# Kernel optimization log

Hardware: AMD Instinct MI355X
Metric: run time of the kernel (lower is better)

## Reference

```python
import jax, jax.numpy as jnp
import numpy as np
from jax import lax

# --- static config (matches init_kwargs) ---
K_NAT, P_NAT, NHEAD, DM, L = 5, 2, 8, 128, 3
PK, OV, STRIDE = 4, 2, 2          # patcher kernel / overlap / stride = PK-OV
PPAD = PK - OV                    # circular pad for patcher/depatcher crop
RK, RC = 5, 12                    # res layer kernel, hidden channels = 3*4
DN = ('NCHW', 'OIHW', 'NCHW')


def setup_inputs() -> dict:
    key = jax.random.key(0)
    ks = jax.random.split(key, 16)
    B, C, H, W = 2, 3, 256, 256
    rn = lambda k, shape, s=0.02: jax.random.normal(k, shape, jnp.float32) * s
    return {
        'x': jax.random.normal(ks[0], (B, C, H, W), jnp.float32),
        'pos_w': jax.random.uniform(ks[1], (C, H, W), jnp.float32) + 0.5,
        'pos_b': jax.random.uniform(ks[2], (C, H, W), jnp.float32) - 0.5,
        'patch_w': rn(ks[3], (DM, C, PK, PK), 0.05),
        'patch_b': jnp.zeros((DM,), jnp.float32),
        'ln1_g': jnp.ones((L, DM), jnp.float32),
        'ln1_b': jnp.zeros((L, DM), jnp.float32),
        'qkv_w': rn(ks[4], (L, 3 * DM, DM)),
        'qkv_b': jnp.zeros((L, 3 * DM), jnp.float32),
        'rpb': rn(ks[5], (L, NHEAD, 2 * K_NAT - 1, 2 * K_NAT - 1)),
        'proj_w': rn(ks[6], (L, DM, DM)),
        'proj_b': jnp.zeros((L, DM), jnp.float32),
        'ln2_g': jnp.ones((L, DM), jnp.float32),
        'ln2_b': jnp.zeros((L, DM), jnp.float32),
        'fc1_w': rn(ks[7], (L, 4 * DM, DM)),
        'fc1_b': jnp.zeros((L, 4 * DM), jnp.float32),
        'fc2_w': rn(ks[8], (L, DM, 4 * DM)),
        'fc2_b': jnp.zeros((L, DM), jnp.float32),
        'depatch_w': rn(ks[9], (DM, C, PK, PK), 0.05),   # ConvTranspose2d weight (Cin,Cout,kh,kw)
        'depatch_b': jnp.zeros((C,), jnp.float32),
        'res_cv1_w': rn(ks[10], (RC, C, RK, RK), 0.05),
        'res_cv1_b': jnp.zeros((RC,), jnp.float32),
        'res_cv2_w': rn(ks[11], (C, RC, 1, 1), 0.05),
        'res_cv2_b': jnp.zeros((C,), jnp.float32),
    }


def _layer_norm(x, g, b):
    m = x.mean(-1, keepdims=True)
    v = x.var(-1, keepdims=True)
    return (x - m) * lax.rsqrt(v + 1e-5) * g + b


def _nat_block(x, ln1_g, ln1_b, qkv_w, qkv_b, rpb, proj_w, proj_b,
               ln2_g, ln2_b, fc1_w, fc1_b, fc2_w, fc2_b):
    # x: (B,H,W,C). NATLayer: LN -> circular pad by k//2 -> NA -> crop -> residual -> LN -> MLP -> residual.
    # After padding, every kept (interior) pixel has a full centered kxk neighborhood,
    # so we compute q only at interior positions and gather kxk K/V windows from the padded map.
    B, H, W, C = x.shape
    k, p, h = K_NAT, P_NAT, NHEAD
    dh = C // h
    y = _layer_norm(x, ln1_g, ln1_b)
    y = jnp.pad(y, ((0, 0), (p, p), (p, p), (0, 0)), mode='wrap')  # circular
    qkv = y @ qkv_w.T + qkv_b                                      # (B,H+2p,W+2p,3C)
    q, kk, vv = jnp.split(qkv, 3, axis=-1)
    q = q[:, p:p + H, p:p + W].reshape(B, H, W, h, dh) * (dh ** -0.5)
    def win(t):
        t = t.reshape(B, H + 2 * p, W + 2 * p, h, dh)
        return jnp.stack([t[:, i:i + H, j:j + W]
                          for i in range(k) for j in range(k)], axis=3)  # (B,H,W,k*k,h,dh)
    kw, vw = win(kk), win(vv)
    bias = rpb[:, p:p + k, p:p + k].reshape(h, k * k)  # centered slice of (2k-1,2k-1) RPB
    logits = jnp.einsum('bxyhd,bxynhd->bxyhn', q, kw) + bias
    a = jax.nn.softmax(logits, axis=-1)
    o = jnp.einsum('bxyhn,bxynhd->bxyhd', a, vw).reshape(B, H, W, C)
    x = x + (o @ proj_w.T + proj_b)
    y = _layer_norm(x, ln2_g, ln2_b)
    y = jax.nn.leaky_relu(y @ fc1_w.T + fc1_b) @ fc2_w.T + fc2_b
    return x + y


def _forward(x, pos_w, pos_b, patch_w, patch_b, ln1_g, ln1_b, qkv_w, qkv_b,
             rpb, proj_w, proj_b, ln2_g, ln2_b, fc1_w, fc1_b, fc2_w, fc2_b,
             depatch_w, depatch_b, res_cv1_w, res_cv1_b, res_cv2_w, res_cv2_b):
    # positional embedding (dropout is identity, p=0)
    x = x * pos_w + pos_b
    # OverlapConvPatcher: circular pad by (PK-OV), conv kernel PK stride PK-OV -> (B,129,129,DM)
    xp = jnp.pad(x, ((0, 0), (0, 0), (PPAD, PPAD), (PPAD, PPAD)), mode='wrap')
    f = lax.conv_general_dilated(xp, patch_w, (STRIDE, STRIDE), 'VALID',
                                 dimension_numbers=DN) + patch_b[None, :, None, None]
    f = f.transpose(0, 2, 3, 1)
    for i in range(L):
        f = _nat_block(f, ln1_g[i], ln1_b[i], qkv_w[i], qkv_b[i], rpb[i],
                       proj_w[i], proj_b[i], ln2_g[i], ln2_b[i],
                       fc1_w[i], fc1_b[i], fc2_w[i], fc2_b[i])
    # OverlapDeconvDepatcher: ConvTranspose2d (kernel PK, stride PK-OV), crop PPAD border
    f = f.transpose(0, 3, 1, 2)
    wf = jnp.flip(depatch_w, (2, 3)).transpose(1, 0, 2, 3)  # (Cout,Cin,kh,kw)
    y = lax.conv_general_dilated(f, wf, (1, 1), [(PK - 1, PK - 1)] * 2,
                                 lhs_dilation=(STRIDE, STRIDE),
                                 dimension_numbers=DN) + depatch_b[None, :, None, None]
    y = y[:, :, PPAD:-PPAD, PPAD:-PPAD]  # (B,3,256,256)
    # ResLayer: circular-pad same conv 5x5 -> leaky_relu -> 1x1 conv -> residual
    yp = jnp.pad(y, ((0, 0), (0, 0), (RK // 2, RK // 2), (RK // 2, RK // 2)), mode='wrap')
    r = lax.conv_general_dilated(yp, res_cv1_w, (1, 1), 'VALID',
                                 dimension_numbers=DN) + res_cv1_b[None, :, None, None]
    r = jax.nn.leaky_relu(r)
    r = lax.conv_general_dilated(r, res_cv2_w, (1, 1), 'VALID',
                                 dimension_numbers=DN) + res_cv2_b[None, :, None, None]
    return y + r


def reference(x, pos_w, pos_b, patch_w, patch_b, ln1_g, ln1_b, qkv_w, qkv_b,
              rpb, proj_w, proj_b, ln2_g, ln2_b, fc1_w, fc1_b, fc2_w, fc2_b,
              depatch_w, depatch_b, res_cv1_w, res_cv1_b, res_cv2_w, res_cv2_b):
    return _forward(x, pos_w, pos_b, patch_w, patch_b, ln1_g, ln1_b, qkv_w, qkv_b,
                    rpb, proj_w, proj_b, ln2_g, ln2_b, fc1_w, fc1_b, fc2_w, fc2_b,
                    depatch_w, depatch_b, res_cv1_w, res_cv1_b, res_cv2_w, res_cv2_b)
```

## Files before the change

kernel.cpp:

```cpp
#include <hip/hip_runtime.h>
#include <hip/hip_bf16.h>
#include <math.h>

#define HF 129
#define WF 129
#define BDIM 2
#define TOK (BDIM*HF*WF)
#define DMOD 128

typedef __attribute__((ext_vector_type(8))) short short8;
typedef __attribute__((ext_vector_type(8))) unsigned short ushort8;
typedef __attribute__((ext_vector_type(4))) float f32x4;

__device__ __forceinline__ float leaky(float v){ return v > 0.f ? v : 0.01f*v; }
__device__ __forceinline__ float bf2f(unsigned short u){ return __uint_as_float(((unsigned int)u) << 16); }
__device__ __forceinline__ unsigned int f2bf(float f){
    unsigned int u = __float_as_uint(f);
    return (u + 0x7fff + ((u >> 16) & 1)) >> 16;
}

#define NQ 147456
#define NPJ 49152
#define N1 196608
#define N2 196608
#define NPAT 8192
#define NDEP 8192
__global__ __launch_bounds__(256) void prep_weights(
    const float* __restrict__ qkv_w, const float* __restrict__ proj_w,
    const float* __restrict__ fc1_w, const float* __restrict__ fc2_w,
    const float* __restrict__ patch_w, const float* __restrict__ dep_w,
    __hip_bfloat16* __restrict__ wq, __hip_bfloat16* __restrict__ wp,
    __hip_bfloat16* __restrict__ w1, __hip_bfloat16* __restrict__ w2,
    __hip_bfloat16* __restrict__ wpat, __hip_bfloat16* __restrict__ wdep,
    float* __restrict__ zero64)
{
    int off = blockIdx.x*256 + threadIdx.x;
    if (off < NQ) { wq[off] = __float2bfloat16(qkv_w[off]); return; } off -= NQ;
    if (off < NPJ){ wp[off] = __float2bfloat16(proj_w[off]); return; } off -= NPJ;
    if (off < N1) { w1[off] = __float2bfloat16(fc1_w[off]); return; } off -= N1;
    if (off < N2) { w2[off] = __float2bfloat16(fc2_w[off]); return; } off -= N2;
    if (off < NPAT){ int r = off>>6, e = off&63;
        wpat[off] = __float2bfloat16(e < 48 ? patch_w[r*48 + e] : 0.f); return; } off -= NPAT;
    if (off < NDEP){ int e = off>>7, d = off&127;
        wdep[off] = __float2bfloat16(e < 48 ? dep_w[d*48 + e] : 0.f); return; } off -= NDEP;
    if (off < 64) zero64[off] = 0.f;
}

__global__ __launch_bounds__(256) void im2col_kernel(
    const float* __restrict__ x, const float* __restrict__ pos_w, const float* __restrict__ pos_b,
    __hip_bfloat16* __restrict__ G)
{
    __shared__ float xs[12][260];
    int blk = blockIdx.x;
    int b = blk / HF, oh = blk - b*HF;
    int tid = threadIdx.x;
    #pragma unroll
    for (int it = 0; it < 3; ++it) {
        int p = it*4 + (tid >> 6);
        int c = p >> 2, r = p & 3;
        int h = (oh*2 + r - 2 + 256) & 255;
        int w4 = (tid & 63) * 4;
        float4 xv  = *(const float4*)(x     + ((size_t)(b*3 + c)*256 + h)*256 + w4);
        float4 pwv = *(const float4*)(pos_w + ((size_t)c*256 + h)*256 + w4);
        float4 pbv = *(const float4*)(pos_b + ((size_t)c*256 + h)*256 + w4);
        float4 o; o.x = xv.x*pwv.x + pbv.x; o.y = xv.y*pwv.y + pbv.y;
        o.z = xv.z*pwv.z + pbv.z; o.w = xv.w*pwv.w + pbv.w;
        *(float4*)&xs[p][w4] = o;
    }
    __syncthreads();
    int e = tid & 63, og = tid >> 6;
    int c = e >> 4, k = e & 15, kh = k >> 2, kw = k & 3;
    int p = c*4 + kh;
    unsigned short* Grow = (unsigned short*)G + (size_t)blk*WF*64;
    for (int ow = og; ow < WF; ow += 4) {
        unsigned short v = 0;
        if (e < 48) {
            int col = (ow*2 + kw - 2 + 256) & 255;
            v = (unsigned short)f2bf(xs[p][col]);
        }
        Grow[ow*64 + e] = v;
    }
}

template<int ACT, int RES, int OUTF, int LNE>
__global__ __launch_bounds__(256) void gemmF_kernel(
    const __hip_bfloat16* __restrict__ A, const __hip_bfloat16* __restrict__ W,
    const float* __restrict__ bias, const float* __restrict__ lng, const float* __restrict__ lnb,
    __hip_bfloat16* __restrict__ Cbf, float* __restrict__ Cf,
    __hip_bfloat16* __restrict__ yl, int M, int N, int K)
{
    __shared__ __align__(16) char As[64*128];
    __shared__ __align__(16) char Ws[128*128];
    __shared__ float2 lnred[64][2];
    int tid = threadIdx.x;
    int bm = blockIdx.x*64, bn = blockIdx.y*128;
    int lane = tid & 63, wid = tid >> 6;
    int wr = (wid >> 1)*32, wc = (wid & 1)*64;
    int lrow = lane & 15, lq = lane >> 4;
    int srow = tid >> 3, scg = tid & 7;
    int swz = (lrow & 7) << 4;
    int awo0 = ((srow     )*128 + scg*16) ^ ((srow&7)<<4);
    int awo1 = ((srow + 32)*128 + scg*16) ^ ((srow&7)<<4);

    bool v0 = (bm + srow) < M, v1 = (bm + srow + 32) < M;
    const __hip_bfloat16* a0p = A + (size_t)(bm + srow)*K + scg*8;
    const __hip_bfloat16* a1p = A + (size_t)(bm + srow + 32)*K + scg*8;
    const __hip_bfloat16* wp0 = W + (size_t)(bn + srow)*K + scg*8;

    f32x4 acc[2][4] = {};
    for (int k0 = 0; k0 < K; k0 += 64) {
        int4 va0 = {}, va1 = {};
        if (v0) va0 = *(const int4*)(a0p + k0);
        if (v1) va1 = *(const int4*)(a1p + k0);
        int4 vw0 = *(const int4*)(wp0 + k0);
        int4 vw1 = *(const int4*)(wp0 + (size_t)32*K + k0);
        int4 vw2 = *(const int4*)(wp0 + (size_t)64*K + k0);
        int4 vw3 = *(const int4*)(wp0 + (size_t)96*K + k0);
        __syncthreads();
        *(int4*)(As + awo0) = va0;
        *(int4*)(As + awo1) = va1;
        *(int4*)(Ws + awo0) = vw0;
        *(int4*)(Ws + awo1) = vw1;
        *(int4*)(Ws + (((srow+64)*128 + scg*16) ^ ((srow&7)<<4))) = vw2;
        *(int4*)(Ws + (((srow+96)*128 + scg*16) ^ ((srow&7)<<4))) = vw3;
        __syncthreads();
        #pragma unroll
        for (int ks = 0; ks < 2; ++ks) {
            int kb = ks*64;
            short8 af[2], bf[4];
            #pragma unroll
            for (int mi = 0; mi < 2; ++mi)
                af[mi] = *(const short8*)(As + (((wr + mi*16 + lrow)*128 + kb + lq*16) ^ swz));
            #pragma unroll
            for (int ni = 0; ni < 4; ++ni)
                bf[ni] = *(const short8*)(Ws + (((wc + ni*16 + lrow)*128 + kb + lq*16) ^ swz));
            #pragma unroll
            for (int mi = 0; mi < 2; ++mi)
                #pragma unroll
                for (int ni = 0; ni < 4; ++ni)
                    acc[mi][ni] = __builtin_amdgcn_mfma_f32_16x16x32_bf16(af[mi], bf[ni], acc[mi][ni], 0, 0, 0);
        }
    }
    float bcol[4];
    #pragma unroll
    for (int ni = 0; ni < 4; ++ni) bcol[ni] = bias[bn + wc + ni*16 + lrow];
    #pragma unroll
    for (int mi = 0; mi < 2; ++mi) {
        #pragma unroll
        for (int r = 0; r < 4; ++r) {
            int row = bm + wr + mi*16 + lq*4 + r;
            bool vrow = row < M;
            #pragma unroll
            for (int ni = 0; ni < 4; ++ni) {
                float v = acc[mi][ni][r] + bcol[ni];
                if (ACT) v = leaky(v);
                if (RES || OUTF) {
                    int col = wc + ni*16 + lrow;
                    size_t idx = (size_t)row*128 + col;
                    if (RES) { float old = vrow ? Cf[idx] : 0.f; v += old; }
                    if (vrow) Cf[idx] = v;
                } else {
                    int col = bn + wc + ni*16 + lrow;
                    if (vrow) Cbf[(size_t)row*N + col] = __float2bfloat16(v);
                }
                acc[mi][ni][r] = v;
            }
        }
    }
    if (LNE) {
        float sa[8], ssa[8];
        #pragma unroll
        for (int mi = 0; mi < 2; ++mi)
            #pragma unroll
            for (int r = 0; r < 4; ++r) {
                float s = 0.f, ss = 0.f;
                #pragma unroll
                for (int ni = 0; ni < 4; ++ni) { float v = acc[mi][ni][r]; s += v; ss += v*v; }
                sa[mi*4+r] = s; ssa[mi*4+r] = ss;
            }
        #pragma unroll
        for (int m = 1; m < 16; m <<= 1) {
            #pragma unroll
            for (int i = 0; i < 8; ++i) { sa[i] += __shfl_xor(sa[i], m); ssa[i] += __shfl_xor(ssa[i], m); }
        }
        if (lrow == 0) {
            #pragma unroll
            for (int i = 0; i < 8; ++i)
                lnred[wr + (i>>2)*16 + lq*4 + (i&3)][wc>>6] = make_float2(sa[i], ssa[i]);
        }
        __syncthreads();
        float gcol[4], bbcol[4];
        #pragma unroll
        for (int ni = 0; ni < 4; ++ni) {
            gcol[ni] = lng[wc + ni*16 + lrow];
            bbcol[ni] = lnb[wc + ni*16 + lrow];
        }
        #pragma unroll
        for (int mi = 0; mi < 2; ++mi) {
            #pragma unroll
            for (int r = 0; r < 4; ++r) {
                int rl = wr + mi*16 + lq*4 + r;
                int row = bm + rl;
                if (row >= M) continue;
                float2 h0 = lnred[rl][0], h1 = lnred[rl][1];
                float mean = (h0.x + h1.x) * (1.f/128.f);
                float var = (h0.y + h1.y) * (1.f/128.f) - mean*mean;
                float inv = rsqrtf(var + 1e-5f);
                #pragma unroll
                for (int ni = 0; ni < 4; ++ni) {
                    int col = wc + ni*16 + lrow;
                    float yv = (acc[mi][ni][r] - mean)*inv*gcol[ni] + bbcol[ni];
                    yl[(size_t)row*128 + col] = __float2bfloat16(yv);
                }
            }
        }
    }
}

__global__ __launch_bounds__(256) void attn_tile_kernel(
    const __hip_bfloat16* __restrict__ qkv, const float* __restrict__ rpb,
    __hip_bfloat16* __restrict__ o)
{
    __shared__ __align__(16) char Kl[96*256];
    __shared__ __align__(16) char Vl[96*256];
    int blk = blockIdx.x;
    int b = blk / (17*33);
    int rem = blk - b*(17*33);
    int tyi = rem / 33, txi = rem - tyi*33;
    int y0 = tyi*8, x0 = txi*4;
    int tid = threadIdx.x;

    #pragma unroll
    for (int it = 0; it < 12; ++it) {
        int u = tid + it*256;
        int wtok = u >> 5;
        int half = (u >> 4) & 1;
        int c = u & 15;
        int wy = wtok >> 3, wx = wtok & 7;
        int gy = y0 + wy - 2; gy += (gy < 0) ? HF : 0; gy -= (gy >= HF) ? HF : 0;
        int gx = x0 + wx - 2; gx += (gx < 0) ? WF : 0; gx -= (gx >= WF) ? WF : 0;
        size_t tok = (size_t)(b*HF + gy)*WF + gx;
        int4 v = *(const int4*)(qkv + tok*384 + 128 + half*128 + c*8);
        char* dst = half ? Vl : Kl;
        *(int4*)(dst + wtok*256 + ((c*16) ^ ((wtok & 7) << 4))) = v;
    }
    __syncthreads();

    {
        int tloc = tid >> 3;
        int head = tid & 7;
        int ty = tloc >> 2, tx = tloc & 3;
        int gy = y0 + ty, gx = x0 + tx;
        bool valid = (gy < HF) && (gx < WF);
        int cy = valid ? gy : HF-1, cx = valid ? gx : WF-1;
        size_t tok = (size_t)(b*HF + cy)*WF + cx;
        const ushort8* qp = (const ushort8*)(qkv + tok*384 + head*16);
        float q[16];
        {
            ushort8 u0 = qp[0], u1 = qp[1];
            #pragma unroll
            for (int i = 0; i < 8; ++i) { q[i] = bf2f(u0[i])*0.25f; q[i+8] = bf2f(u1[i])*0.25f; }
        }
        const float* rb = rpb + head*81;
        float logits[25];
        float mx = -1e30f;
        #pragma unroll
        for (int di = 0; di < 5; ++di) {
            #pragma unroll
            for (int dj = 0; dj < 5; ++dj) {
                int wtok = (ty + di)*8 + tx + dj;
                int sw = (wtok & 7) << 4;
                ushort8 k0 = *(const ushort8*)(Kl + wtok*256 + ((head*32) ^ sw));
                ushort8 k1 = *(const ushort8*)(Kl + wtok*256 + ((head*32 + 16) ^ sw));
                float d = 0.f;
                #pragma unroll
                for (int i = 0; i < 8; ++i) d += q[i]*bf2f(k0[i]) + q[i+8]*bf2f(k1[i]);
                d += rb[(di+2)*9 + dj + 2];
                logits[di*5 + dj] = d;
                mx = fmaxf(mx, d);
            }
        }
        float s = 0.f;
        #pragma unroll
        for (int n = 0; n < 25; ++n) { float p = __expf(logits[n]-mx); logits[n] = p; s += p; }
        float invs = 1.f/s;
        float outv[16] = {};
        #pragma unroll
        for (int di = 0; di < 5; ++di) {
            #pragma unroll
            for (int dj = 0; dj < 5; ++dj) {
                int wtok = (ty + di)*8 + tx + dj;
                int sw = (wtok & 7) << 4;
                ushort8 v0 = *(const ushort8*)(Vl + wtok*256 + ((head*32) ^ sw));
                ushort8 v1 = *(const ushort8*)(Vl + wtok*256 + ((head*32 + 16) ^ sw));
                float p = logits[di*5 + dj];
                #pragma unroll
                for (int i = 0; i < 8; ++i) { outv[i] += p*bf2f(v0[i]); outv[i+8] += p*bf2f(v1[i]); }
            }
        }
        if (valid) {
            int4 w0, w1;
            unsigned int pk[8];
            #pragma unroll
            for (int i = 0; i < 8; ++i)
                pk[i] = f2bf(outv[2*i]*invs) | (f2bf(outv[2*i+1]*invs) << 16);
            w0.x = (int)pk[0]; w0.y = (int)pk[1]; w0.z = (int)pk[2]; w0.w = (int)pk[3];
            w1.x = (int)pk[4]; w1.y = (int)pk[5]; w1.z = (int)pk[6]; w1.w = (int)pk[7];
            __hip_bfloat16* op = o + tok*128 + head*16;
            *(int4*)op = w0;
            *(int4*)(op + 8) = w1;
        }
    }
}

template<int ACT, int RES, int OUTF, int A32>
__global__ __launch_bounds__(256) void mgemm_kernel(
    const void* __restrict__ Av, const __hip_bfloat16* __restrict__ W,
    const float* __restrict__ bias, __hip_bfloat16* __restrict__ Cbf,
    float* __restrict__ Cres, int M, int N, int K)
{
    __shared__ __align__(16) char As[64*128];
    __shared__ __align__(16) char Ws[64*128];
    int tid = threadIdx.x;
    int bm = blockIdx.x*64, bn = blockIdx.y*64;
    int lane = tid & 63, wid = tid >> 6;
    int wm = (wid >> 1)*32, wn = (wid & 1)*32;
    int lrow = lane & 15, lq = lane >> 4;
    int srow = tid >> 3, scg = tid & 7;
    int wo0 = ((srow     )*128 + scg*16) ^ ((srow&7)<<4);
    int wo1 = ((srow + 32)*128 + scg*16) ^ ((srow&7)<<4);
    int swz = (lrow & 7) << 4;
    int baseA0 = (wm + lrow     )*128 + lq*16;
    int baseA1 = (wm + 16 + lrow)*128 + lq*16;
    int baseB0 = (wn + lrow     )*128 + lq*16;
    int baseB1 = (wn + 16 + lrow)*128 + lq*16;

    f32x4 acc[2][2] = {};
    bool v0 = (bm + srow) < M, v1 = (bm + srow + 32) < M;
    const __hip_bfloat16* a0p = (const __hip_bfloat16*)Av + (size_t)(bm + srow)*K + scg*8;
    const __hip_bfloat16* a1p = (const __hip_bfloat16*)Av + (size_t)(bm + srow + 32)*K + scg*8;
    const float* a0pf = (const float*)Av + (size_t)(bm + srow)*K + scg*8;
    const float* a1pf = (const float*)Av + (size_t)(bm + srow + 32)*K + scg*8;
    const __hip_bfloat16* w0p = W + (size_t)(bn + srow)*K + scg*8;
    const __hip_bfloat16* w1p = W + (size_t)(bn + srow + 32)*K + scg*8;

    for (int k0 = 0; k0 < K; k0 += 64) {
        int4 va0 = {}, va1 = {};
        if (A32) {
            if (v0) {
                float4 p0 = *(const float4*)(a0pf + k0);
                float4 p1 = *(const float4*)(a0pf + k0 + 4);
                va0.x = (int)(f2bf(p0.x) | (f2bf(p0.y) << 16)); va0.y = (int)(f2bf(p0.z) | (f2bf(p0.w) << 16));
                va0.z = (int)(f2bf(p1.x) | (f2bf(p1.y) << 16)); va0.w = (int)(f2bf(p1.z) | (f2bf(p1.w) << 16));
            }
            if (v1) {
                float4 p0 = *(const float4*)(a1pf + k0);
                float4 p1 = *(const float4*)(a1pf + k0 + 4);
                va1.x = (int)(f2bf(p0.x) | (f2bf(p0.y) << 16)); va1.y = (int)(f2bf(p0.z) | (f2bf(p0.w) << 16));
                va1.z = (int)(f2bf(p1.x) | (f2bf(p1.y) << 16)); va1.w = (int)(f2bf(p1.z) | (f2bf(p1.w) << 16));
            }
        } else {
            if (v0) va0 = *(const int4*)(a0p + k0);
            if (v1) va1 = *(const int4*)(a1p + k0);
        }
        int4 vw0 = *(const int4*)(w0p + k0);
        int4 vw1 = *(const int4*)(w1p + k0);
        __syncthreads();
        *(int4*)(As + wo0) = va0;
        *(int4*)(As + wo1) = va1;
        *(int4*)(Ws + wo0) = vw0;
        *(int4*)(Ws + wo1) = vw1;
        __syncthreads();
        #pragma unroll
        for (int ks = 0; ks < 2; ++ks) {
            int kb = ks*64;
            short8 a0 = *(const short8*)(As + ((baseA0 + kb) ^ swz));
            short8 a1 = *(const short8*)(As + ((baseA1 + kb) ^ swz));
            short8 b0 = *(const short8*)(Ws + ((baseB0 + kb) ^ swz));
            short8 b1 = *(const short8*)(Ws + ((baseB1 + kb) ^ swz));
            acc[0][0] = __builtin_amdgcn_mfma_f32_16x16x32_bf16(a0, b0, acc[0][0], 0, 0, 0);
            acc[0][1] = __builtin_amdgcn_mfma_f32_16x16x32_bf16(a0, b1, acc[0][1], 0, 0, 0);
            acc[1][0] = __builtin_amdgcn_mfma_f32_16x16x32_bf16(a1, b0, acc[1][0], 0, 0, 0);
            acc[1][1] = __builtin_amdgcn_mfma_f32_16x16x32_bf16(a1, b1, acc[1][1], 0, 0, 0);
        }
    }
    float bv0 = bias[bn + wn + lrow];
    float bv1 = bias[bn + wn + 16 + lrow];
    #pragma unroll
    for (int mi = 0; mi < 2; ++mi) {
        #pragma unroll
        for (int r = 0; r < 4; ++r) {
            int row = bm + wm + mi*16 + lq*4 + r;
            if (row >= M) continue;
            #pragma unroll
            for (int ni = 0; ni < 2; ++ni) {
                float v = acc[mi][ni][r] + (ni ? bv1 : bv0);
                if (ACT == 1) v = leaky(v);
                int col = bn + wn + ni*16 + lrow;
                if (RES)       Cres[(size_t)row*N + col] += v;
                else if (OUTF) Cres[(size_t)row*N + col] = v;
                else           Cbf[(size_t)row*N + col] = __float2bfloat16(v);
            }
        }
    }
}

__global__ __launch_bounds__(256) void degather_kernel(const float* __restrict__ G,
    const float* __restrict__ db, float* __restrict__ yimg)
{
    int idx = blockIdx.x*256 + threadIdx.x;
    int b = idx >> 16;
    int pix = idx & 65535;
    int i = pix >> 8, j = pix & 255;
    int fh0 = i >> 1, fw0 = j >> 1;
    size_t r00 = ((size_t)(b*HF + fh0)*WF + fw0)*64;
    size_t r01 = r00 + 64;
    size_t r10 = r00 + (size_t)WF*64;
    size_t r11 = r10 + 64;
    int wr0 = (2 + (i & 1))*4, wr1 = (i & 1)*4;
    int wc0 = 2 + (j & 1), wc1 = (j & 1);
    #pragma unroll
    for (int c = 0; c < 3; ++c) {
        int e = c*16;
        float v = db[c]
                + G[r00 + e + wr0 + wc0] + G[r01 + e + wr0 + wc1]
                + G[r10 + e + wr1 + wc0] + G[r11 + e + wr1 + wc1];
        yimg[((size_t)(b*3 + c) << 16) + pix] = v;
    }
}

__global__ __launch_bounds__(256) void res_kernel(const float* __restrict__ y,
    const float* __restrict__ w1, const float* __restrict__ b1,
    const float* __restrict__ w2, const float* __restrict__ b2, float* __restrict__ out)
{
    int idx = blockIdx.x*256 + threadIdx.x;
    int b = idx >> 16;
    int pix = idx & 65535;
    int i = pix >> 8, j = pix & 255;
    float yv[3][5][5];
    #pragma unroll
    for (int c = 0; c < 3; ++c) {
        #pragma unroll
        for (int u = 0; u < 5; ++u) {
            int ii = (i + u - 2 + 256) & 255;
            #pragma unroll
            for (int v = 0; v < 5; ++v) {
                int jj = (j + v - 2 + 256) & 255;
                yv[c][u][v] = y[((size_t)(b*3 + c)*256 + ii)*256 + jj];
            }
        }
    }
    float r1[12];
    #pragma unroll
    for (int rc = 0; rc < 12; ++rc) {
        float a = b1[rc];
        #pragma unroll
        for (int c = 0; c < 3; ++c)
            #pragma unroll
            for (int u = 0; u < 5; ++u)
                #pragma unroll
                for (int v = 0; v < 5; ++v)
                    a += yv[c][u][v] * w1[rc*75 + c*25 + u*5 + v];
        r1[rc] = leaky(a);
    }
    #pragma unroll
    for (int c = 0; c < 3; ++c) {
        float a = b2[c];
        #pragma unroll
        for (int rc = 0; rc < 12; ++rc) a += r1[rc]*w2[c*12 + rc];
        out[((size_t)(b*3 + c)*256 + i)*256 + j] = yv[c][2][2] + a;
    }
}

extern "C" void kernel_launch(void* const* d_in, const int* in_sizes, int n_in,
                              void* d_out, int out_size, void* d_ws, size_t ws_size,
                              hipStream_t stream)
{
    const float* x      = (const float*)d_in[0];
    const float* pos_w  = (const float*)d_in[1];
    const float* pos_b  = (const float*)d_in[2];
    const float* patch_w= (const float*)d_in[3];
    const float* patch_b= (const float*)d_in[4];
    const float* ln1_g  = (const float*)d_in[5];
    const float* ln1_b  = (const float*)d_in[6];
    const float* qkv_w  = (const float*)d_in[7];
    const float* qkv_b  = (const float*)d_in[8];
    const float* rpb    = (const float*)d_in[9];
    const float* proj_w = (const float*)d_in[10];
    const float* proj_b = (const float*)d_in[11];
    const float* ln2_g  = (const float*)d_in[12];
    const float* ln2_b  = (const float*)d_in[13];
    const float* fc1_w  = (const float*)d_in[14];
    const float* fc1_b  = (const float*)d_in[15];
    const float* fc2_w  = (const float*)d_in[16];
    const float* fc2_b  = (const float*)d_in[17];
    const float* dep_w  = (const float*)d_in[18];
    const float* dep_b  = (const float*)d_in[19];
    const float* rc1_w  = (const float*)d_in[20];
    const float* rc1_b  = (const float*)d_in[21];
    const float* rc2_w  = (const float*)d_in[22];
    const float* rc2_b  = (const float*)d_in[23];

    const size_t SZ = (size_t)TOK * 128;
    char* w = (char*)d_ws;
    float* f            = (float*)w;            w += SZ*4;
    __hip_bfloat16* yln = (__hip_bfloat16*)w;   w += SZ*2;
    __hip_bfloat16* ao  = (__hip_bfloat16*)w;   w += SZ*2;
    __hip_bfloat16* qkvb= (__hip_bfloat16*)w;   w += (size_t)TOK*384*2;
    __hip_bfloat16* hb  = (__hip_bfloat16*)w;   w += (size_t)TOK*512*2;
    float* yimg         = (float*)w;            w += (size_t)BDIM*3*65536*4;
    __hip_bfloat16* wq  = (__hip_bfloat16*)w;   w += (size_t)NQ*2;
    __hip_bfloat16* wp  = (__hip_bfloat16*)w;   w += (size_t)NPJ*2;
    __hip_bfloat16* w1  = (__hip_bfloat16*)w;   w += (size_t)N1*2;
    __hip_bfloat16* w2  = (__hip_bfloat16*)w;   w += (size_t)N2*2;
    __hip_bfloat16* wpat= (__hip_bfloat16*)w;   w += (size_t)NPAT*2;
    __hip_bfloat16* wdep= (__hip_bfloat16*)w;   w += (size_t)NDEP*2;
    float* zero64       = (float*)w;            w += 64*4;

    __hip_bfloat16* icol = qkvb;
    float* G             = (float*)hb;

    const int PREP_TOT = NQ + NPJ + N1 + N2 + NPAT + NDEP + 64;
    prep_weights<<<(PREP_TOT + 255)/256, 256, 0, stream>>>(
        qkv_w, proj_w, fc1_w, fc2_w, patch_w, dep_w, wq, wp, w1, w2, wpat, wdep, zero64);

    im2col_kernel<<<BDIM*HF, 256, 0, stream>>>(x, pos_w, pos_b, icol);

    const int GM = (TOK + 63)/64;
    const int NTILE = 17*33*BDIM;

    gemmF_kernel<0,0,1,1><<<dim3(GM,1), 256, 0, stream>>>(icol, wpat, patch_b,
        ln1_g, ln1_b, nullptr, f, yln, TOK, 128, 64);

    for (int l = 0; l < 3; ++l) {
        gemmF_kernel<0,0,0,0><<<dim3(GM,3), 256, 0, stream>>>(yln, wq + (size_t)l*384*128,
            qkv_b + l*384, nullptr, nullptr, qkvb, nullptr, nullptr, TOK, 384, 128);
        attn_tile_kernel<<<NTILE, 256, 0, stream>>>(qkvb, rpb + l*8*81, ao);
        gemmF_kernel<0,1,0,1><<<dim3(GM,1), 256, 0, stream>>>(ao, wp + (size_t)l*128*128,
            proj_b + l*128, ln2_g + l*128, ln2_b + l*128, nullptr, f, yln, TOK, 128, 128);
        gemmF_kernel<1,0,0,0><<<dim3(GM,4), 256, 0, stream>>>(yln, w1 + (size_t)l*512*128,
            fc1_b + l*512, nullptr, nullptr, hb, nullptr, nullptr, TOK, 512, 128);
        if (l < 2)
            gemmF_kernel<0,1,0,1><<<dim3(GM,1), 256, 0, stream>>>(hb, w2 + (size_t)l*128*512,
                fc2_b + l*128, ln1_g + (l+1)*128, ln1_b + (l+1)*128, nullptr, f, yln, TOK, 128, 512);
        else
            gemmF_kernel<0,1,0,0><<<dim3(GM,1), 256, 0, stream>>>(hb, w2 + (size_t)l*128*512,
                fc2_b + l*128, nullptr, nullptr, nullptr, f, nullptr, TOK, 128, 512);
    }

    mgemm_kernel<0,0,1,1><<<dim3(GM,1), 256, 0, stream>>>(f, wdep, zero64,
        nullptr, G, TOK, 64, 128);
    degather_kernel<<<512, 256, 0, stream>>>(G, dep_b, yimg);

    res_kernel<<<512, 256, 0, stream>>>(yimg, rc1_w, rc1_b, rc2_w, rc2_b, (float*)d_out);
}
```

Baseline: 365.0 us.

## Compute neighborhood attention tiles with MFMA dense window scores and masking

Replaces the scalar per-thread neighborhood attention with an MFMA version. Each wave computes dense QK scores between 32 queries and the whole 96-token window, masks entries outside each query's 5x5 neighborhood, adds the relative position bias staged in shared memory, and does softmax with cross-lane shuffles. The probabilities are written to shared memory as bf16, and a second MFMA multiplies them by V, which is stored transposed in LDS. This trades scalar FMA work for matrix-core throughput, but computes many masked scores that are wasted and adds extra LDS traffic and a bf16 rounding of the probabilities.

```diff
diff --git a/kernel.cpp b/kernel.cpp
--- a/kernel.cpp
+++ b/kernel.cpp
@@ -7,6 +7,7 @@
 #define BDIM 2
 #define TOK (BDIM*HF*WF)
 #define DMOD 128
+#define VTP 104
 
 typedef __attribute__((ext_vector_type(8))) short short8;
 typedef __attribute__((ext_vector_type(8))) unsigned short ushort8;
@@ -217,98 +218,164 @@
     }
 }
 
-__global__ __launch_bounds__(256) void attn_tile_kernel(
+__global__ __launch_bounds__(256) void attn_mfma_kernel(
     const __hip_bfloat16* __restrict__ qkv, const float* __restrict__ rpb,
     __hip_bfloat16* __restrict__ o)
 {
     __shared__ __align__(16) char Kl[96*256];
-    __shared__ __align__(16) char Vl[96*256];
+    __shared__ __align__(16) char Vt[128*VTP*2];
+    __shared__ __align__(16) char Pl[4][32*VTP*2];
+    __shared__ float rpbl[8*81];
     int blk = blockIdx.x;
     int b = blk / (17*33);
     int rem = blk - b*(17*33);
     int tyi = rem / 33, txi = rem - tyi*33;
     int y0 = tyi*8, x0 = txi*4;
     int tid = threadIdx.x;
-
-    #pragma unroll
-    for (int it = 0; it < 12; ++it) {
+    int lane = tid & 63, wid = tid >> 6;
+    int lrow = lane & 15, lq = lane >> 4;
+
+    for (int u = tid; u < 648; u += 256) rpbl[u] = rpb[u];
+
+    #pragma unroll
+    for (int it = 0; it < 6; ++it) {
         int u = tid + it*256;
-        int wtok = u >> 5;
-        int half = (u >> 4) & 1;
-        int c = u & 15;
+        int wtok = u >> 4, c = u & 15;
         int wy = wtok >> 3, wx = wtok & 7;
         int gy = y0 + wy - 2; gy += (gy < 0) ? HF : 0; gy -= (gy >= HF) ? HF : 0;
         int gx = x0 + wx - 2; gx += (gx < 0) ? WF : 0; gx -= (gx >= WF) ? WF : 0;
-        size_t tok = (size_t)(b*HF + gy)*WF + gx;
-        int4 v = *(const int4*)(qkv + tok*384 + 128 + half*128 + c*8);
-        char* dst = half ? Vl : Kl;
-        *(int4*)(dst + wtok*256 + ((c*16) ^ ((wtok & 7) << 4))) = v;
+        size_t tk = (size_t)(b*HF + gy)*WF + gx;
+        int4 v = *(const int4*)(qkv + tk*384 + 128 + c*8);
+        *(int4*)(Kl + wtok*256 + ((c*16) ^ ((wtok & 7) << 4))) = v;
+    }
+    #pragma unroll
+    for (int it = 0; it < 6; ++it) {
+        int u = tid + it*256;
+        int c = u / 96, wtok = u - c*96;
+        int wy = wtok >> 3, wx = wtok & 7;
+        int gy = y0 + wy - 2; gy += (gy < 0) ? HF : 0; gy -= (gy >= HF) ? HF : 0;
+        int gx = x0 + wx - 2; gx += (gx < 0) ? WF : 0; gx -= (gx >= WF) ? WF : 0;
+        size_t tk = (size_t)(b*HF + gy)*WF + gx;
+        ushort8 v = *(const ushort8*)(qkv + tk*384 + 256 + c*8);
+        unsigned short* dst = (unsigned short*)Vt + (c*8)*VTP + wtok;
+        #pragma unroll
+        for (int j = 0; j < 8; ++j) dst[j*VTP] = v[j];
     }
     __syncthreads();
 
-    {
-        int tloc = tid >> 3;
-        int head = tid & 7;
-        int ty = tloc >> 2, tx = tloc & 3;
-        int gy = y0 + ty, gx = x0 + tx;
-        bool valid = (gy < HF) && (gx < WF);
-        int cy = valid ? gy : HF-1, cx = valid ? gx : WF-1;
-        size_t tok = (size_t)(b*HF + cy)*WF + cx;
-        const ushort8* qp = (const ushort8*)(qkv + tok*384 + head*16);
-        float q[16];
-        {
-            ushort8 u0 = qp[0], u1 = qp[1];
-            #pragma unroll
-            for (int i = 0; i < 8; ++i) { q[i] = bf2f(u0[i])*0.25f; q[i+8] = bf2f(u1[i])*0.25f; }
-        }
-        const float* rb = rpb + head*81;
-        float logits[25];
-        float mx = -1e30f;
-        #pragma unroll
-        for (int di = 0; di < 5; ++di) {
-            #pragma unroll
-            for (int dj = 0; dj < 5; ++dj) {
-                int wtok = (ty + di)*8 + tx + dj;
-                int sw = (wtok & 7) << 4;
-                ushort8 k0 = *(const ushort8*)(Kl + wtok*256 + ((head*32) ^ sw));
-                ushort8 k1 = *(const ushort8*)(Kl + wtok*256 + ((head*32 + 16) ^ sw));
-                float d = 0.f;
-                #pragma unroll
-                for (int i = 0; i < 8; ++i) d += q[i]*bf2f(k0[i]) + q[i+8]*bf2f(k1[i]);
-                d += rb[(di+2)*9 + dj + 2];
-                logits[di*5 + dj] = d;
-                mx = fmaxf(mx, d);
-            }
-        }
-        float s = 0.f;
-        #pragma unroll
-        for (int n = 0; n < 25; ++n) { float p = __expf(logits[n]-mx); logits[n] = p; s += p; }
-        float invs = 1.f/s;
-        float outv[16] = {};
-        #pragma unroll
-        for (int di = 0; di < 5; ++di) {
-            #pragma unroll
-            for (int dj = 0; dj < 5; ++dj) {
-                int wtok = (ty + di)*8 + tx + dj;
-                int sw = (wtok & 7) << 4;
-                ushort8 v0 = *(const ushort8*)(Vl + wtok*256 + ((head*32) ^ sw));
-                ushort8 v1 = *(const ushort8*)(Vl + wtok*256 + ((head*32 + 16) ^ sw));
-                float p = logits[di*5 + dj];
-                #pragma unroll
-                for (int i = 0; i < 8; ++i) { outv[i] += p*bf2f(v0[i]); outv[i+8] += p*bf2f(v1[i]); }
-            }
-        }
-        if (valid) {
-            int4 w0, w1;
-            unsigned int pk[8];
-            #pragma unroll
-            for (int i = 0; i < 8; ++i)
-                pk[i] = f2bf(outv[2*i]*invs) | (f2bf(outv[2*i+1]*invs) << 16);
-            w0.x = (int)pk[0]; w0.y = (int)pk[1]; w0.z = (int)pk[2]; w0.w = (int)pk[3];
-            w1.x = (int)pk[4]; w1.y = (int)pk[5]; w1.z = (int)pk[6]; w1.w = (int)pk[7];
-            __hip_bfloat16* op = o + tok*128 + head*16;
-            *(int4*)op = w0;
-            *(int4*)(op + 8) = w1;
+    char* myP = Pl[wid];
+    #pragma unroll
+    for (int hh = 0; hh < 2; ++hh) {
+        int h = wid + hh*4;
+        short8 aq[2];
+        #pragma unroll
+        for (int mi = 0; mi < 2; ++mi) {
+            int q = mi*16 + lrow;
+            int ty = q >> 2, tx = q & 3;
+            int gy = y0 + ty, gx = x0 + tx;
+            int cy = gy < HF ? gy : HF-1, cx = gx < WF ? gx : WF-1;
+            size_t tk = (size_t)(b*HF + cy)*WF + cx;
+            short8 v = {};
+            if (lq < 2) v = *(const short8*)(qkv + tk*384 + h*16 + lq*8);
+            aq[mi] = v;
+        }
+        f32x4 sc[2][6];
+        #pragma unroll
+        for (int ni = 0; ni < 6; ++ni) {
+            int krow = ni*16 + lrow;
+            short8 bk = *(const short8*)(Kl + krow*256 + ((h*32 + (lq&1)*16) ^ ((krow&7)<<4)));
+            f32x4 zz = {0.f,0.f,0.f,0.f};
+            sc[0][ni] = __builtin_amdgcn_mfma_f32_16x16x32_bf16(aq[0], bk, zz, 0, 0, 0);
+            sc[1][ni] = __builtin_amdgcn_mfma_f32_16x16x32_bf16(aq[1], bk, zz, 0, 0, 0);
+        }
+        int wxv = lrow & 7;
+        int wyb = lrow >> 3;
+        #pragma unroll
+        for (int mi = 0; mi < 2; ++mi) {
+            int tyq = mi*4 + lq;
+            #pragma unroll
+            for (int ni = 0; ni < 6; ++ni) {
+                int dy = ni*2 + wyb - tyq;
+                bool vdy = (dy >= 0) && (dy <= 4);
+                int base = (dy + 2)*9 + wxv + 2;
+                int cb = base < 3 ? 3 : (base > 80 ? 80 : base);
+                const float* bp = rpbl + h*81 + cb - 3;
+                float b0 = bp[0], b1 = bp[1], b2 = bp[2], b3 = bp[3];
+                float bias_r[4] = {b3, b2, b1, b0};
+                #pragma unroll
+                for (int r = 0; r < 4; ++r) {
+                    int dx = wxv - r;
+                    bool ok = vdy && (dx >= 0) && (dx <= 4);
+                    float s = sc[mi][ni][r]*0.25f + bias_r[r];
+                    sc[mi][ni][r] = ok ? s : -1e30f;
+                }
+            }
+        }
+        float mx[8];
+        #pragma unroll
+        for (int mi = 0; mi < 2; ++mi)
+            #pragma unroll
+            for (int r = 0; r < 4; ++r) {
+                float m = sc[mi][0][r];
+                #pragma unroll
+                for (int ni = 1; ni < 6; ++ni) m = fmaxf(m, sc[mi][ni][r]);
+                mx[mi*4 + r] = m;
+            }
+        #pragma unroll
+        for (int msk = 1; msk < 16; msk <<= 1)
+            #pragma unroll
+            for (int i = 0; i < 8; ++i) mx[i] = fmaxf(mx[i], __shfl_xor(mx[i], msk));
+        float sum[8] = {};
+        #pragma unroll
+        for (int mi = 0; mi < 2; ++mi)
+            #pragma unroll
+            for (int ni = 0; ni < 6; ++ni)
+                #pragma unroll
+                for (int r = 0; r < 4; ++r) {
+                    float p = __expf(sc[mi][ni][r] - mx[mi*4 + r]);
+                    sc[mi][ni][r] = p;
+                    sum[mi*4 + r] += p;
+                }
+        #pragma unroll
+        for (int msk = 1; msk < 16; msk <<= 1)
+            #pragma unroll
+            for (int i = 0; i < 8; ++i) sum[i] += __shfl_xor(sum[i], msk);
+        float inv[8];
+        #pragma unroll
+        for (int i = 0; i < 8; ++i) inv[i] = 1.f / sum[i];
+        #pragma unroll
+        for (int mi = 0; mi < 2; ++mi)
+            #pragma unroll
+            for (int ni = 0; ni < 6; ++ni)
+                #pragma unroll
+                for (int r = 0; r < 4; ++r) {
+                    int q = mi*16 + lq*4 + r;
+                    int w = ni*16 + lrow;
+                    ((unsigned short*)myP)[q*VTP + w] =
+                        (unsigned short)f2bf(sc[mi][ni][r]*inv[mi*4 + r]);
+                }
+        f32x4 ov[2] = {};
+        #pragma unroll
+        for (int kk = 0; kk < 3; ++kk) {
+            short8 vb = *(const short8*)(Vt + (h*16 + lrow)*(VTP*2) + kk*64 + lq*16);
+            #pragma unroll
+            for (int mi = 0; mi < 2; ++mi) {
+                short8 pa = *(const short8*)(myP + (mi*16 + lrow)*(VTP*2) + kk*64 + lq*16);
+                ov[mi] = __builtin_amdgcn_mfma_f32_16x16x32_bf16(pa, vb, ov[mi], 0, 0, 0);
+            }
+        }
+        #pragma unroll
+        for (int mi = 0; mi < 2; ++mi) {
+            int tyq = mi*4 + lq;
+            int gy = y0 + tyq;
+            #pragma unroll
+            for (int r = 0; r < 4; ++r) {
+                int gx = x0 + r;
+                if (gy < HF && gx < WF) {
+                    size_t tk = (size_t)(b*HF + gy)*WF + gx;
+                    ((unsigned short*)o)[tk*128 + h*16 + lrow] = (unsigned short)f2bf(ov[mi][r]);
+                }
+            }
         }
     }
 }
@@ -535,7 +602,7 @@
     for (int l = 0; l < 3; ++l) {
         gemmF_kernel<0,0,0,0><<<dim3(GM,3), 256, 0, stream>>>(yln, wq + (size_t)l*384*128,
             qkv_b + l*384, nullptr, nullptr, qkvb, nullptr, nullptr, TOK, 384, 128);
-        attn_tile_kernel<<<NTILE, 256, 0, stream>>>(qkvb, rpb + l*8*81, ao);
+        attn_mfma_kernel<<<NTILE, 256, 0, stream>>>(qkvb, rpb + l*8*81, ao);
         gemmF_kernel<0,1,0,1><<<dim3(GM,1), 256, 0, stream>>>(ao, wp + (size_t)l*128*128,
             proj_b + l*128, ln2_g + l*128, ln2_b + l*128, nullptr, f, yln, TOK, 128, 128);
         gemmF_kernel<1,0,0,0><<<dim3(GM,4), 256, 0, stream>>>(yln, w1 + (size_t)l*512*128,
```

New measurement: 344.3 us. -5.7%, faster.
